# Kernel optimization log

Measured on AMD Instinct MI355X. Metric: run time of the kernel, lower is better.

## Reference

```python
import jax, jax.numpy as jnp
import numpy as np

B, NPG, FANOUT = 32, 1024, 4       # graphs, nodes per graph, tree fan-out
H = 128                            # x_size == h_size
NUM_LAYERS = 4
A, BCAPS = 8, 8                    # TreeCaps a, b
DCC, N_CLASSES = 16, 50
ROUTING_ITER = 3
TYPE_VOCAB, TOKEN_VOCAB = 1000, 30000
EPS = 1e-10


def _build_forest():
    # parent of node i (i>0) is (i-1)//FANOUT; node 0 is root. Same tree per graph.
    child = np.arange(1, NPG)
    parent = (child - 1) // FANOUT
    pos = ((child - 1) % FANOUT).astype(np.float32)           # position in parent's mailbox
    cnt = np.bincount(parent, minlength=NPG).astype(np.float32)
    k = cnt[parent]                                           # child count of each edge's parent
    denom = np.maximum(k - 1.0, 1.0)
    lw = np.where(k == 1.0, 1.0, (k - 1.0 - pos) / denom).astype(np.float32)
    rw = np.where(k == 1.0, 0.0, pos / denom).astype(np.float32)
    offs = (np.arange(B) * NPG)[:, None]
    src = (child[None, :] + offs).reshape(-1).astype(np.int32)
    dst = (parent[None, :] + offs).reshape(-1).astype(np.int32)
    return src, dst, np.tile(lw, B), np.tile(rw, B), np.tile(cnt > 0, B)


def setup_inputs() -> dict:
    key = jax.random.key(0)
    ks = jax.random.split(key, 9)
    src, dst, lw, rw, has_children = _build_forest()
    N = B * NPG
    u = lambda k, s: jax.random.uniform(k, s, jnp.float32, -0.1, 0.1)
    return {
        "type_ids": jax.random.randint(ks[0], (N,), 0, TYPE_VOCAB, dtype=jnp.int32),
        "token_ids": jax.random.randint(ks[1], (N,), 0, TOKEN_VOCAB, dtype=jnp.int32),
        "src": jnp.asarray(src), "dst": jnp.asarray(dst),
        "lw": jnp.asarray(lw), "rw": jnp.asarray(rw),
        "has_children": jnp.asarray(has_children),
        "type_emb": jax.random.normal(ks[2], (TYPE_VOCAB, H - H // 2), jnp.float32),
        "token_emb": jax.random.normal(ks[3], (TOKEN_VOCAB, H // 2), jnp.float32),
        "W_left": u(ks[4], (NUM_LAYERS, H, H)),
        "W_right": u(ks[5], (NUM_LAYERS, H, H)),
        "W_top": u(ks[6], (NUM_LAYERS, H, H)),
        "b_conv": u(ks[7], (NUM_LAYERS, H)),
        "Wjm": 0.01 * jax.random.normal(ks[8], (A * H, DCC, N_CLASSES, NUM_LAYERS), jnp.float32),
    }


def squash(x, axis=-1):
    sq = jnp.sum(x * x, axis=axis, keepdims=True)
    return x * (sq / (1.0 + sq) / (jnp.sqrt(sq + EPS) + 1e-8))


def _vts_routing(uu):
    # uu: [NPG, H, L]  (one graph's primary capsules)
    l2 = jnp.sum(uu.reshape(NPG, -1) ** 2, axis=1)
    _, top_b = jax.lax.top_k(l2, BCAPS)
    u_i = jax.lax.stop_gradient(uu[top_b].reshape(-1, NUM_LAYERS))  # [BCAPS*H, L]
    _, top_a = jax.lax.top_k(l2, A)
    v_j = uu[top_a].reshape(-1, NUM_LAYERS)                         # [A*H, L]
    alpha = jnp.zeros((BCAPS * H, A * H), uu.dtype)
    for _ in range(ROUTING_ITER):
        alpha = alpha + u_i @ v_j.T
        beta = jax.nn.softmax(alpha, axis=-1)
        v_j = beta.T @ u_i
    return squash(v_j)                                              # [A*H, L]


def _dynamic_routing(SC, Wjm):
    # SC: [B, A*H, L], Wjm: [A*H, DCC, S, L]
    v = jnp.einsum('ncsm,bnm->bnsc', Wjm, SC)
    v_stop = jax.lax.stop_gradient(v)
    delta = jnp.zeros(SC.shape[:2] + (N_CLASSES,), SC.dtype)
    z = None
    for r in range(ROUTING_ITER):
        gamma = jax.nn.softmax(delta, axis=-1)
        vv = v if r == ROUTING_ITER - 1 else v_stop
        z = squash(jnp.einsum('bns,bnsc->bsc', gamma, vv))
        if r < ROUTING_ITER - 1:
            delta = delta + jnp.einsum('bnsc,bsc->bns', v_stop, z)
    return z                                                        # [B, S, DCC]


def reference(type_ids, token_ids, src, dst, lw, rw, has_children,
              type_emb, token_emb, W_left, W_right, W_top, b_conv, Wjm):
    h = jnp.concatenate([type_emb[type_ids], token_emb[token_ids]], axis=1)  # [N, H]
    N = h.shape[0]
    feats = []
    for l in range(NUM_LAYERS):
        ch = h[src]                                                 # [E, H] gather children
        msg = (ch @ W_left[l]) * lw[:, None] + (ch @ W_right[l]) * rw[:, None]
        children = jax.ops.segment_sum(msg, dst, num_segments=N)
        new_h = jax.nn.relu(children + h @ W_top[l] + b_conv[l][None, :])
        h = jnp.where(has_children[:, None], new_h, h)              # leaves keep old h
        feats.append(h)
    layer_feats = jnp.stack(feats, axis=-1)                         # [N, H, L]
    SC = jax.vmap(_vts_routing)(layer_feats.reshape(B, NPG, H, NUM_LAYERS))
    z = _dynamic_routing(SC, Wjm)
    logit = jnp.sqrt(jnp.sum(z * z, axis=-1) + EPS)                 # [B, S]
    return (logit, logit)
```

## Files before the change

### kernel.cpp

```cpp
#include <hip/hip_runtime.h>


#define BG      32
#define NPG     1024
#define HH      128
#define NLAY    4
#define INT_PG  256
#define M_INT   8192
#define NN      32768
#define EPG     1023
#define DCC     16
#define NS      50

__global__ void k_embed(const int* __restrict__ tids, const int* __restrict__ kids,
                        const float* __restrict__ temb, const float* __restrict__ kemb,
                        float* __restrict__ h) {
  int idx = blockIdx.x * 256 + threadIdx.x;
  int n = idx >> 5, c4 = idx & 31;
  float4 v;
  if (c4 < 16) v = *(const float4*)(temb + tids[n] * 64 + c4 * 4);
  else         v = *(const float4*)(kemb + kids[n] * 64 + (c4 - 16) * 4);
  *(float4*)(h + n * 128 + c4 * 4) = v;
}

__global__ void k_gather(const float* __restrict__ h, const int* __restrict__ src,
                         const float* __restrict__ lw, const float* __restrict__ rw,
                         float* __restrict__ hl, float* __restrict__ hr) {
  int idx = blockIdx.x * 256 + threadIdx.x;
  int p = idx >> 5, c4 = idx & 31;
  int g = p >> 8, pl = p & 255;
  float4 al = make_float4(0.f, 0.f, 0.f, 0.f);
  float4 ar = make_float4(0.f, 0.f, 0.f, 0.f);
  for (int j = 0; j < 4; ++j) {
    int cc = 4 * pl + 1 + j;
    if (cc < NPG) {
      int e = g * EPG + cc - 1;
      int child = src[e];
      float lv = lw[e], rv = rw[e];
      float4 hv = *(const float4*)(h + child * 128 + c4 * 4);
      al.x = fmaf(lv, hv.x, al.x); al.y = fmaf(lv, hv.y, al.y);
      al.z = fmaf(lv, hv.z, al.z); al.w = fmaf(lv, hv.w, al.w);
      ar.x = fmaf(rv, hv.x, ar.x); ar.y = fmaf(rv, hv.y, ar.y);
      ar.z = fmaf(rv, hv.z, ar.z); ar.w = fmaf(rv, hv.w, ar.w);
    }
  }
  *(float4*)(hl + p * 128 + c4 * 4) = al;
  *(float4*)(hr + p * 128 + c4 * 4) = ar;
}

__global__ __launch_bounds__(256) void k_conv(
    const float* __restrict__ hl, const float* __restrict__ hr,
    float* __restrict__ h,
    const float* __restrict__ Wl, const float* __restrict__ Wr,
    const float* __restrict__ Wt, const float* __restrict__ bias,
    float* __restrict__ feat) {
  __shared__ float Ws[32][128];
  __shared__ float AsT[32][40];
  int tid = threadIdx.x;
  int tx = tid & 31, ty = tid >> 5;
  int rowBase = blockIdx.x * 32;
  int nodeBase = ((rowBase >> 8) << 10) + (rowBase & 255);
  float acc[4][4] = {};
  int sr = tid >> 3, sc4 = (tid & 7) * 4;

  for (int kc = 0; kc < 12; ++kc) {
    int ssel = kc >> 2, kcol = (kc & 3) * 32;
    const float* ap = (ssel == 0) ? (hl + rowBase * 128)
                    : (ssel == 1) ? (hr + rowBase * 128)
                                  : (h + nodeBase * 128);
    const float* wsrc = ((ssel == 0) ? Wl : (ssel == 1) ? Wr : Wt) + kcol * 128;
    float4 av = *(const float4*)(ap + sr * 128 + kcol + sc4);
    float4 wv0, wv1, wv2, wv3;
    {
      int f0 = tid, f1 = tid + 256, f2 = tid + 512, f3 = tid + 768;
      wv0 = *(const float4*)(wsrc + (f0 >> 5) * 128 + (f0 & 31) * 4);
      wv1 = *(const float4*)(wsrc + (f1 >> 5) * 128 + (f1 & 31) * 4);
      wv2 = *(const float4*)(wsrc + (f2 >> 5) * 128 + (f2 & 31) * 4);
      wv3 = *(const float4*)(wsrc + (f3 >> 5) * 128 + (f3 & 31) * 4);
    }
    __syncthreads();
    AsT[sc4 + 0][sr] = av.x; AsT[sc4 + 1][sr] = av.y;
    AsT[sc4 + 2][sr] = av.z; AsT[sc4 + 3][sr] = av.w;
    {
      int f0 = tid, f1 = tid + 256, f2 = tid + 512, f3 = tid + 768;
      *(float4*)&Ws[f0 >> 5][(f0 & 31) * 4] = wv0;
      *(float4*)&Ws[f1 >> 5][(f1 & 31) * 4] = wv1;
      *(float4*)&Ws[f2 >> 5][(f2 & 31) * 4] = wv2;
      *(float4*)&Ws[f3 >> 5][(f3 & 31) * 4] = wv3;
    }
    __syncthreads();
    #pragma unroll
    for (int kk = 0; kk < 32; ++kk) {
      float4 wv = *(float4*)&Ws[kk][tx * 4];
      float4 av2 = *(float4*)&AsT[kk][ty * 4];
      float aa[4] = {av2.x, av2.y, av2.z, av2.w};
      float ww[4] = {wv.x, wv.y, wv.z, wv.w};
      #pragma unroll
      for (int i = 0; i < 4; ++i)
        #pragma unroll
        for (int j = 0; j < 4; ++j)
          acc[i][j] = fmaf(aa[i], ww[j], acc[i][j]);
    }
  }
  float4 bv = *(const float4*)(bias + tx * 4);
  float bb[4] = {bv.x, bv.y, bv.z, bv.w};
  #pragma unroll
  for (int i = 0; i < 4; ++i) {
    int r = ty * 4 + i;
    float4 o = make_float4(fmaxf(acc[i][0] + bb[0], 0.f),
                           fmaxf(acc[i][1] + bb[1], 0.f),
                           fmaxf(acc[i][2] + bb[2], 0.f),
                           fmaxf(acc[i][3] + bb[3], 0.f));
    *(float4*)(feat + (rowBase + r) * 128 + tx * 4) = o;
    *(float4*)(h + (nodeBase + r) * 128 + tx * 4) = o;
  }
}

__global__ void k_l2(const float* __restrict__ h, const float* __restrict__ feat,
                     float* __restrict__ l2) {
  int wid = (blockIdx.x * 256 + threadIdx.x) >> 6;
  int lane = threadIdx.x & 63;
  int g = wid >> 10, local = wid & 1023;
  float s = 0.f;
  if (local >= INT_PG) {
    const float* p = h + wid * 128;
    float a = p[lane], b = p[lane + 64];
    s = (a * a + b * b) * 4.f;
  } else {
    int row = (g * INT_PG + local) * 128;
    #pragma unroll
    for (int l = 0; l < 4; ++l) {
      const float* p = feat + l * (M_INT * 128) + row;
      float a = p[lane], b = p[lane + 64];
      s += a * a + b * b;
    }
  }
  #pragma unroll
  for (int off = 32; off; off >>= 1) s += __shfl_down(s, off);
  if (lane == 0) l2[wid] = s;
}

__global__ void k_topk(const float* __restrict__ l2, int* __restrict__ sel) {
  __shared__ unsigned long long keys[1024];
  __shared__ unsigned long long red[256];
  int g = blockIdx.x, tid = threadIdx.x;
  for (int i = tid; i < 1024; i += 256) {
    unsigned vb = __float_as_uint(l2[g * 1024 + i]);
    keys[i] = ((unsigned long long)vb << 32) | (unsigned)(~i);
  }
  __syncthreads();
  for (int r = 0; r < 8; ++r) {
    unsigned long long best = 0ULL;
    for (int i = tid; i < 1024; i += 256) {
      unsigned long long k = keys[i];
      best = (k > best) ? k : best;
    }
    red[tid] = best;
    __syncthreads();
    for (int st = 128; st; st >>= 1) {
      if (tid < st) {
        unsigned long long a = red[tid], b = red[tid + st];
        red[tid] = (b > a) ? b : a;
      }
      __syncthreads();
    }
    if (tid == 0) {
      unsigned long long k = red[0];
      int idx = (int)(~(unsigned)(k & 0xffffffffu));
      sel[g * 8 + r] = idx;
      keys[idx] = 0ULL;
    }
    __syncthreads();
  }
}

__global__ void k_buildU(const float* __restrict__ h, const float* __restrict__ feat,
                         const int* __restrict__ sel,
                         float* __restrict__ U, float* __restrict__ Vsum) {
  int idx = blockIdx.x * 256 + threadIdx.x;
  int g = idx >> 10, rank = (idx >> 7) & 7, hh = idx & 127;
  int local = sel[g * 8 + rank];
  float4 v;
  if (local >= INT_PG) {
    float x = h[(g * NPG + local) * 128 + hh];
    v = make_float4(x, x, x, x);
  } else {
    int row = (g * INT_PG + local) * 128 + hh;
    v.x = feat[row];
    v.y = feat[M_INT * 128 + row];
    v.z = feat[2 * M_INT * 128 + row];
    v.w = feat[3 * M_INT * 128 + row];
  }
  int o = g * 1024 + rank * 128 + hh;
  ((float4*)U)[o] = v;
  ((float4*)Vsum)[o] = v;
}

__global__ __launch_bounds__(1024) void k_vtsA(const float* __restrict__ U,
                                               const float* __restrict__ Vsum,
                                               float* __restrict__ mw, float* __restrict__ sw) {
  __shared__ float4 Vs[1024];
  __shared__ float2 red[1024];
  int g = blockIdx.x >> 3, rb = (blockIdx.x & 7) * 128;
  int tid = threadIdx.x, l = tid & 63, p = tid >> 6;
  Vs[tid] = ((const float4*)Vsum)[g * 1024 + tid];
  __syncthreads();
  float4 u0 = ((const float4*)U)[g * 1024 + rb + l];
  float4 u1 = ((const float4*)U)[g * 1024 + rb + 64 + l];
  int j0 = p * 64;
  float m0 = -3.4e38f, m1 = -3.4e38f;
  for (int j = j0; j < j0 + 64; ++j) {
    float4 v = Vs[j];
    float a0 = u0.x * v.x + u0.y * v.y + u0.z * v.z + u0.w * v.w;
    float a1 = u1.x * v.x + u1.y * v.y + u1.z * v.z + u1.w * v.w;
    m0 = fmaxf(m0, a0); m1 = fmaxf(m1, a1);
  }
  red[tid] = make_float2(m0, m1);
  __syncthreads();
  #pragma unroll
  for (int st = 512; st >= 64; st >>= 1) {
    if (tid < st) {
      float2 a = red[tid], b = red[tid + st];
      red[tid] = make_float2(fmaxf(a.x, b.x), fmaxf(a.y, b.y));
    }
    __syncthreads();
  }
  float2 mm = red[l];
  __syncthreads();
  float s0 = 0.f, s1 = 0.f;
  for (int j = j0; j < j0 + 64; ++j) {
    float4 v = Vs[j];
    float a0 = u0.x * v.x + u0.y * v.y + u0.z * v.z + u0.w * v.w;
    float a1 = u1.x * v.x + u1.y * v.y + u1.z * v.z + u1.w * v.w;
    s0 += __expf(a0 - mm.x);
    s1 += __expf(a1 - mm.y);
  }
  red[tid] = make_float2(s0, s1);
  __syncthreads();
  #pragma unroll
  for (int st = 512; st >= 64; st >>= 1) {
    if (tid < st) {
      float2 a = red[tid], b = red[tid + st];
      red[tid] = make_float2(a.x + b.x, a.y + b.y);
    }
    __syncthreads();
  }
  if (tid < 64) {
    float2 ss = red[tid];
    mw[g * 1024 + rb + tid] = mm.x;
    mw[g * 1024 + rb + 64 + tid] = mm.y;
    sw[g * 1024 + rb + tid] = ss.x;
    sw[g * 1024 + rb + 64 + tid] = ss.y;
  }
}

__global__ __launch_bounds__(1024) void k_vtsB(const float* __restrict__ U,
                                               float* __restrict__ Vsum,
                                               const float* __restrict__ mw,
                                               const float* __restrict__ sw,
                                               float* __restrict__ SCT, int last) {
  __shared__ float4 Us[1024];
  __shared__ float2 ms[1024];
  __shared__ float4 par[1024];
  int g = blockIdx.x >> 3, cb = (blockIdx.x & 7) * 128;
  int tid = threadIdx.x, l = tid & 63, p = tid >> 6;
  Us[tid] = ((const float4*)U)[g * 1024 + tid];
  ms[tid] = make_float2(mw[g * 1024 + tid], 1.0f / sw[g * 1024 + tid]);
  __syncthreads();
  float4 v0 = ((const float4*)Vsum)[g * 1024 + cb + l];
  float4 v1 = ((const float4*)Vsum)[g * 1024 + cb + 64 + l];
  float4 acc0 = make_float4(0.f, 0.f, 0.f, 0.f);
  float4 acc1 = make_float4(0.f, 0.f, 0.f, 0.f);
  int i0 = p * 64;
  for (int i = i0; i < i0 + 64; ++i) {
    float4 uu = Us[i];
    float2 st = ms[i];
    float a0 = uu.x * v0.x + uu.y * v0.y + uu.z * v0.z + uu.w * v0.w;
    float a1 = uu.x * v1.x + uu.y * v1.y + uu.z * v1.z + uu.w * v1.w;
    float w0 = __expf(a0 - st.x) * st.y;
    float w1 = __expf(a1 - st.x) * st.y;
    acc0.x = fmaf(w0, uu.x, acc0.x); acc0.y = fmaf(w0, uu.y, acc0.y);
    acc0.z = fmaf(w0, uu.z, acc0.z); acc0.w = fmaf(w0, uu.w, acc0.w);
    acc1.x = fmaf(w1, uu.x, acc1.x); acc1.y = fmaf(w1, uu.y, acc1.y);
    acc1.z = fmaf(w1, uu.z, acc1.z); acc1.w = fmaf(w1, uu.w, acc1.w);
  }
  par[tid] = acc0;
  __syncthreads();
  #pragma unroll
  for (int st = 512; st >= 64; st >>= 1) {
    if (tid < st) {
      float4 a = par[tid], b = par[tid + st];
      par[tid] = make_float4(a.x + b.x, a.y + b.y, a.z + b.z, a.w + b.w);
    }
    __syncthreads();
  }
  float4 o0;
  if (tid < 64) o0 = par[tid];
  __syncthreads();
  par[tid] = acc1;
  __syncthreads();
  #pragma unroll
  for (int st = 512; st >= 64; st >>= 1) {
    if (tid < st) {
      float4 a = par[tid], b = par[tid + st];
      par[tid] = make_float4(a.x + b.x, a.y + b.y, a.z + b.z, a.w + b.w);
    }
    __syncthreads();
  }
  if (tid < 64) {
    float4 o1 = par[tid];
    int j0c = cb + tid, j1c = cb + 64 + tid;
    if (last) {
      float sq0 = o0.x * o0.x + o0.y * o0.y + o0.z * o0.z + o0.w * o0.w;
      float f0 = (sq0 / (1.f + sq0)) / (sqrtf(sq0 + 1e-10f) + 1e-8f);
      ((float4*)SCT)[j0c * 32 + g] = make_float4(o0.x * f0, o0.y * f0, o0.z * f0, o0.w * f0);
      float sq1 = o1.x * o1.x + o1.y * o1.y + o1.z * o1.z + o1.w * o1.w;
      float f1 = (sq1 / (1.f + sq1)) / (sqrtf(sq1 + 1e-10f) + 1e-8f);
      ((float4*)SCT)[j1c * 32 + g] = make_float4(o1.x * f1, o1.y * f1, o1.z * f1, o1.w * f1);
    } else {
      float4 w0 = ((const float4*)Vsum)[g * 1024 + j0c];
      float4 w1 = ((const float4*)Vsum)[g * 1024 + j1c];
      ((float4*)Vsum)[g * 1024 + j0c] = make_float4(w0.x + o0.x, w0.y + o0.y,
                                                    w0.z + o0.z, w0.w + o0.w);
      ((float4*)Vsum)[g * 1024 + j1c] = make_float4(w1.x + o1.x, w1.y + o1.y,
                                                    w1.z + o1.z, w1.w + o1.w);
    }
  }
}

__global__ void k_transW(const float* __restrict__ Wjm, float* __restrict__ WT) {
  __shared__ float w[3200];
  int n = blockIdx.x, tid = threadIdx.x;
  for (int i = tid; i < 3200; i += 256) w[i] = Wjm[n * 3200 + i];
  __syncthreads();
  for (int i = tid; i < 3200; i += 256) {
    int s = i >> 6, cm = i & 63, cc = cm >> 2, m = cm & 3;
    WT[(s * 1024 + n) * 64 + cm] = w[(cc * NS + s) * 4 + m];
  }
}

__global__ void k_gamma(const float* __restrict__ delta, float* __restrict__ gT) {
  int idx = blockIdx.x * 256 + threadIdx.x;
  int b = idx & 31, n = idx >> 5;
  const float* dp = delta + n * 32 + b;
  float m = -3.4e38f;
  for (int s = 0; s < NS; ++s) m = fmaxf(m, dp[s * 32768]);
  float sum = 0.f;
  for (int s = 0; s < NS; ++s) sum += __expf(dp[s * 32768] - m);
  float inv = 1.0f / sum;
  float* gp = gT + n * 32 + b;
  for (int s = 0; s < NS; ++s) gp[s * 32768] = __expf(dp[s * 32768] - m) * inv;
}

__global__ __launch_bounds__(256) void k_zsweep(const float* __restrict__ WT,
                                                const float* __restrict__ SCT,
                                                const float* __restrict__ gT,
                                                float* __restrict__ accZ, int it0) {
  int sb = blockIdx.x >> 3, nb = blockIdx.x & 7;
  int tid = threadIdx.x;
  int b = tid & 31, ch = tid >> 5;
  int n0 = nb * 128;
  const float4* wt = (const float4*)WT + (sb * 1024 + n0) * 16;
  const float4* sct = (const float4*)SCT + n0 * 32 + b;
  const float* gp = gT + (sb * 1024 + n0) * 32 + b;
  float a0 = 0.f, a1 = 0.f;
  for (int nn = 0; nn < 128; ++nn) {
    float4 w0 = wt[nn * 16 + ch];
    float4 w1 = wt[nn * 16 + ch + 8];
    float4 s4 = sct[nn * 32];
    float gm = it0 ? (1.0f / 50.0f) : gp[nn * 32];
    float t0 = w0.x * s4.x + w0.y * s4.y + w0.z * s4.z + w0.w * s4.w;
    float t1 = w1.x * s4.x + w1.y * s4.y + w1.z * s4.z + w1.w * s4.w;
    a0 = fmaf(gm, t0, a0);
    a1 = fmaf(gm, t1, a1);
  }
  atomicAdd(accZ + (b * NS + sb) * 16 + ch, a0);
  atomicAdd(accZ + (b * NS + sb) * 16 + ch + 8, a1);
}

__global__ void k_squash(const float* __restrict__ accZ, float* __restrict__ z,
                         float* __restrict__ out, int fin) {
  int idx = blockIdx.x * 256 + threadIdx.x;
  if (idx >= 1600) return;
  const float4* a4 = (const float4*)accZ + idx * 4;
  float4 u0 = a4[0], u1 = a4[1], u2 = a4[2], u3 = a4[3];
  float sq = u0.x * u0.x + u0.y * u0.y + u0.z * u0.z + u0.w * u0.w
           + u1.x * u1.x + u1.y * u1.y + u1.z * u1.z + u1.w * u1.w
           + u2.x * u2.x + u2.y * u2.y + u2.z * u2.z + u2.w * u2.w
           + u3.x * u3.x + u3.y * u3.y + u3.z * u3.z + u3.w * u3.w;
  float f = (sq / (1.f + sq)) / (sqrtf(sq + 1e-10f) + 1e-8f);
  if (fin) {
    float lg = sqrtf(sq * f * f + 1e-10f);
    out[idx] = lg;
    out[idx + 1600] = lg;
  } else {
    float4* z4 = (float4*)z + idx * 4;
    z4[0] = make_float4(u0.x * f, u0.y * f, u0.z * f, u0.w * f);
    z4[1] = make_float4(u1.x * f, u1.y * f, u1.z * f, u1.w * f);
    z4[2] = make_float4(u2.x * f, u2.y * f, u2.z * f, u2.w * f);
    z4[3] = make_float4(u3.x * f, u3.y * f, u3.z * f, u3.w * f);
  }
}

__global__ __launch_bounds__(256) void k_dsweep(const float* __restrict__ WT,
                                                const float* __restrict__ SCT,
                                                const float* __restrict__ z,
                                                float* __restrict__ delta, int first) {
  __shared__ float wl[50 * 64];
  __shared__ float4 scl[32];
  int n = blockIdx.x;
  int tid = threadIdx.x;
  for (int i = tid; i < 3200; i += 256)
    wl[i] = WT[((i >> 6) * 1024 + n) * 64 + (i & 63)];
  if (tid < 32) scl[tid] = ((const float4*)SCT)[n * 32 + tid];
  __syncthreads();
  for (int idx = tid; idx < 1600; idx += 256) {
    int s = idx >> 5, b = idx & 31;
    const float4* wp = (const float4*)(wl + s * 64);
    const float4* zp = (const float4*)(z + (b * 50 + s) * 16);
    float4 z0 = zp[0], z1 = zp[1], z2 = zp[2], z3 = zp[3];
    float zs[16] = {z0.x, z0.y, z0.z, z0.w, z1.x, z1.y, z1.z, z1.w,
                    z2.x, z2.y, z2.z, z2.w, z3.x, z3.y, z3.z, z3.w};
    float4 y = make_float4(0.f, 0.f, 0.f, 0.f);
    #pragma unroll
    for (int c = 0; c < 16; ++c) {
      float4 w = wp[c];
      float zc = zs[c];
      y.x = fmaf(zc, w.x, y.x); y.y = fmaf(zc, w.y, y.y);
      y.z = fmaf(zc, w.z, y.z); y.w = fmaf(zc, w.w, y.w);
    }
    float4 sc = scl[b];
    float dd = sc.x * y.x + sc.y * y.y + sc.z * y.z + sc.w * y.w;
    float* dp = delta + (s * 1024 + n) * 32 + b;
    if (first) *dp = dd; else *dp = *dp + dd;
  }
}

extern "C" void kernel_launch(void* const* d_in, const int* in_sizes, int n_in,
                              void* d_out, int out_size, void* d_ws, size_t ws_size,
                              hipStream_t stream) {
  const int*   type_ids  = (const int*)d_in[0];
  const int*   token_ids = (const int*)d_in[1];
  const int*   src       = (const int*)d_in[2];
  const float* lw        = (const float*)d_in[4];
  const float* rw        = (const float*)d_in[5];
  const float* temb      = (const float*)d_in[7];
  const float* kemb      = (const float*)d_in[8];
  const float* Wl        = (const float*)d_in[9];
  const float* Wr        = (const float*)d_in[10];
  const float* Wt        = (const float*)d_in[11];
  const float* bconv     = (const float*)d_in[12];
  const float* Wjm       = (const float*)d_in[13];
  float* out = (float*)d_out;
  char* wsb = (char*)d_ws;

  float* h     = (float*)(wsb + 0);
  float* WT    = (float*)(wsb + 0);
  float* feat  = (float*)(wsb + 16777216);
  float* gT    = (float*)(wsb + 16777216);
  float* delta = (float*)(wsb + 23330816);
  float* accZ  = (float*)(wsb + 29884416);
  float* zbuf  = (float*)(wsb + 29986816);
  float* hl    = (float*)(wsb + 33554432);
  float* hr    = (float*)(wsb + 37748736);
  float* l2b   = (float*)(wsb + 33554432);
  int*   sel   = (int*)  (wsb + 33685504);
  float* U     = (float*)(wsb + 33686528);
  float* Vsum  = (float*)(wsb + 34210816);
  float* mw    = (float*)(wsb + 34735104);
  float* sw    = (float*)(wsb + 34866176);
  float* SCT   = (float*)(wsb + 34997248);

  k_embed<<<4096, 256, 0, stream>>>(type_ids, token_ids, temb, kemb, h);

  for (int l = 0; l < NLAY; ++l) {
    k_gather<<<1024, 256, 0, stream>>>(h, src, lw, rw, hl, hr);
    k_conv<<<256, 256, 0, stream>>>(hl, hr, h,
                                    Wl + l * 16384, Wr + l * 16384, Wt + l * 16384,
                                    bconv + l * 128, feat + l * (M_INT * 128));
  }

  k_l2<<<8192, 256, 0, stream>>>(h, feat, l2b);
  k_topk<<<32, 256, 0, stream>>>(l2b, sel);
  k_buildU<<<128, 256, 0, stream>>>(h, feat, sel, U, Vsum);
  k_transW<<<1024, 256, 0, stream>>>(Wjm, WT);

  for (int it = 0; it < 3; ++it) {
    k_vtsA<<<256, 1024, 0, stream>>>(U, Vsum, mw, sw);
    k_vtsB<<<256, 1024, 0, stream>>>(U, Vsum, mw, sw, SCT, it == 2 ? 1 : 0);
  }

  for (int it = 0; it < 3; ++it) {
    if (it > 0) k_gamma<<<128, 256, 0, stream>>>(delta, gT);
    hipMemsetAsync(accZ, 0, 32 * 50 * 16 * 4, stream);
    k_zsweep<<<400, 256, 0, stream>>>(WT, SCT, gT, accZ, it == 0 ? 1 : 0);
    k_squash<<<7, 256, 0, stream>>>(accZ, zbuf, out, it == 2 ? 1 : 0);
    if (it < 2) k_dsweep<<<1024, 256, 0, stream>>>(WT, SCT, zbuf, delta, it == 0 ? 1 : 0);
  }
}
```

Before: 518.9 us.

## Fuse pipeline into three persistent kernels with software grid barriers

Replaces roughly twenty kernel launches with three persistent kernels: tree conv plus top-k selection, VTS routing, and dynamic routing. Stages are separated by atomic-counter grid barriers instead of launch boundaries. The child gather is fused into the conv kernel, which keeps weighted child sums in registers and drops the hl/hr intermediate buffers and the src indirection. This removes launch overhead and intermediate global traffic, but relies on every block being co-resident, and the spin barriers can serialize work or deadlock if occupancy is insufficient.

Measured after the change: 1.401 ms. 2.7x slower.

```diff
diff --git a/kernel.cpp b/kernel.cpp
--- a/kernel.cpp
+++ b/kernel.cpp
@@ -3,436 +3,475 @@
 
 #define BG      32
 #define NPG     1024
-#define HH      128
 #define NLAY    4
 #define INT_PG  256
 #define M_INT   8192
 #define NN      32768
 #define EPG     1023
-#define DCC     16
 #define NS      50
 
-__global__ void k_embed(const int* __restrict__ tids, const int* __restrict__ kids,
-                        const float* __restrict__ temb, const float* __restrict__ kemb,
-                        float* __restrict__ h) {
-  int idx = blockIdx.x * 256 + threadIdx.x;
-  int n = idx >> 5, c4 = idx & 31;
-  float4 v;
-  if (c4 < 16) v = *(const float4*)(temb + tids[n] * 64 + c4 * 4);
-  else         v = *(const float4*)(kemb + kids[n] * 64 + (c4 - 16) * 4);
-  *(float4*)(h + n * 128 + c4 * 4) = v;
+__device__ __forceinline__ void gbar(unsigned int* bar, unsigned int target) {
+  __syncthreads();
+  if (threadIdx.x == 0) {
+    __threadfence();
+    __hip_atomic_fetch_add(bar, 1u, __ATOMIC_ACQ_REL, __HIP_MEMORY_SCOPE_AGENT);
+    while (__hip_atomic_load(bar, __ATOMIC_ACQUIRE, __HIP_MEMORY_SCOPE_AGENT) < target)
+      __builtin_amdgcn_s_sleep(1);
+  }
+  __syncthreads();
 }
 
-__global__ void k_gather(const float* __restrict__ h, const int* __restrict__ src,
-                         const float* __restrict__ lw, const float* __restrict__ rw,
-                         float* __restrict__ hl, float* __restrict__ hr) {
-  int idx = blockIdx.x * 256 + threadIdx.x;
-  int p = idx >> 5, c4 = idx & 31;
-  int g = p >> 8, pl = p & 255;
-  float4 al = make_float4(0.f, 0.f, 0.f, 0.f);
-  float4 ar = make_float4(0.f, 0.f, 0.f, 0.f);
-  for (int j = 0; j < 4; ++j) {
-    int cc = 4 * pl + 1 + j;
-    if (cc < NPG) {
-      int e = g * EPG + cc - 1;
-      int child = src[e];
-      float lv = lw[e], rv = rw[e];
-      float4 hv = *(const float4*)(h + child * 128 + c4 * 4);
-      al.x = fmaf(lv, hv.x, al.x); al.y = fmaf(lv, hv.y, al.y);
-      al.z = fmaf(lv, hv.z, al.z); al.w = fmaf(lv, hv.w, al.w);
-      ar.x = fmaf(rv, hv.x, ar.x); ar.y = fmaf(rv, hv.y, ar.y);
-      ar.z = fmaf(rv, hv.z, ar.z); ar.w = fmaf(rv, hv.w, ar.w);
-    }
-  }
-  *(float4*)(hl + p * 128 + c4 * 4) = al;
-  *(float4*)(hr + p * 128 + c4 * 4) = ar;
+__global__ __launch_bounds__(256) void k_mega(
+    const int* __restrict__ tids, const int* __restrict__ kids,
+    const float* __restrict__ temb, const float* __restrict__ kemb,
+    const float* __restrict__ lw, const float* __restrict__ rw,
+    const float* __restrict__ Wl, const float* __restrict__ Wr,
+    const float* __restrict__ Wt, const float* __restrict__ bconv,
+    float* __restrict__ h, float* __restrict__ feat,
+    float* __restrict__ l2b, int* __restrict__ sel,
+    float* __restrict__ U, float* __restrict__ Vsum,
+    unsigned int* __restrict__ bar) {
+  __shared__ union {
+    struct { float Ws[32][128]; float AsT[32][36]; } c;
+    struct { unsigned long long keys[1024]; unsigned long long red[256]; } t;
+  } sm;
+  int tid = threadIdx.x, bid = blockIdx.x;
+  int gtid = bid * 256 + tid;
+  unsigned int bt = 0;
+
+  for (int i = gtid; i < NN * 32; i += 65536) {
+    int n = i >> 5, c4 = i & 31;
+    float4 v;
+    if (c4 < 16) v = *(const float4*)(temb + tids[n] * 64 + c4 * 4);
+    else         v = *(const float4*)(kemb + kids[n] * 64 + (c4 - 16) * 4);
+    *(float4*)(h + n * 128 + c4 * 4) = v;
+  }
+  bt += 256; gbar(bar, bt);
+
+  int rowBase = bid * 32;
+  int g = rowBase >> 8, pb = rowBase & 255;
+  int nodeBase = g * 1024 + pb;
+  int tx = tid & 31, ty = tid >> 5;
+  int p8 = tid >> 3, c16 = (tid & 7) * 16;
+
+  for (int l = 0; l < NLAY; ++l) {
+    float av[16], bv[16], cv[16];
+    {
+      int PL = pb + p8;
+      const float* hp = h + (g * 1024 + PL) * 128 + c16;
+      #pragma unroll
+      for (int q = 0; q < 4; ++q) {
+        float4 t4 = *(const float4*)(hp + q * 4);
+        cv[q*4] = t4.x; cv[q*4+1] = t4.y; cv[q*4+2] = t4.z; cv[q*4+3] = t4.w;
+      }
+      #pragma unroll
+      for (int i = 0; i < 16; ++i) { av[i] = 0.f; bv[i] = 0.f; }
+      for (int j = 0; j < 4; ++j) {
+        int cc = 4 * PL + 1 + j;
+        if (cc < 1024) {
+          int e = g * EPG + cc - 1;
+          float lv = lw[e], rv = rw[e];
+          const float* hc = h + (g * 1024 + cc) * 128 + c16;
+          #pragma unroll
+          for (int q = 0; q < 4; ++q) {
+            float4 t4 = *(const float4*)(hc + q * 4);
+            av[q*4]   = fmaf(lv, t4.x, av[q*4]);   bv[q*4]   = fmaf(rv, t4.x, bv[q*4]);
+            av[q*4+1] = fmaf(lv, t4.y, av[q*4+1]); bv[q*4+1] = fmaf(rv, t4.y, bv[q*4+1]);
+            av[q*4+2] = fmaf(lv, t4.z, av[q*4+2]); bv[q*4+2] = fmaf(rv, t4.z, bv[q*4+2]);
+            av[q*4+3] = fmaf(lv, t4.w, av[q*4+3]); bv[q*4+3] = fmaf(rv, t4.w, bv[q*4+3]);
+          }
+        }
+      }
+    }
+    bt += 256; gbar(bar, bt);
+
+    const float* WlL = Wl + l * 16384;
+    const float* WrL = Wr + l * 16384;
+    const float* WtL = Wt + l * 16384;
+    float acc[4][4] = {};
+    for (int kc = 0; kc < 12; ++kc) {
+      int ssel = kc >> 2, koff = (kc & 3) * 32;
+      const float* wsrc = ((ssel == 0) ? WlL : (ssel == 1) ? WrL : WtL) + koff * 128;
+      float4 wv0, wv1, wv2, wv3;
+      {
+        int f0 = tid, f1 = tid + 256, f2 = tid + 512, f3 = tid + 768;
+        wv0 = *(const float4*)(wsrc + (f0 >> 5) * 128 + (f0 & 31) * 4);
+        wv1 = *(const float4*)(wsrc + (f1 >> 5) * 128 + (f1 & 31) * 4);
+        wv2 = *(const float4*)(wsrc + (f2 >> 5) * 128 + (f2 & 31) * 4);
+        wv3 = *(const float4*)(wsrc + (f3 >> 5) * 128 + (f3 & 31) * 4);
+      }
+      __syncthreads();
+      {
+        int f0 = tid, f1 = tid + 256, f2 = tid + 512, f3 = tid + 768;
+        *(float4*)&sm.c.Ws[f0 >> 5][(f0 & 31) * 4] = wv0;
+        *(float4*)&sm.c.Ws[f1 >> 5][(f1 & 31) * 4] = wv1;
+        *(float4*)&sm.c.Ws[f2 >> 5][(f2 & 31) * 4] = wv2;
+        *(float4*)&sm.c.Ws[f3 >> 5][(f3 & 31) * 4] = wv3;
+      }
+      int rel = (tid & 7) - ((kc & 3) << 1);
+      if (rel == 0 || rel == 1) {
+        int kk0 = rel << 4;
+        if (ssel == 0) {
+          #pragma unroll
+          for (int i = 0; i < 16; ++i) sm.c.AsT[kk0 + i][p8] = av[i];
+        } else if (ssel == 1) {
+          #pragma unroll
+          for (int i = 0; i < 16; ++i) sm.c.AsT[kk0 + i][p8] = bv[i];
+        } else {
+          #pragma unroll
+          for (int i = 0; i < 16; ++i) sm.c.AsT[kk0 + i][p8] = cv[i];
+        }
+      }
+      __syncthreads();
+      #pragma unroll
+      for (int kk = 0; kk < 32; ++kk) {
+        float4 wv = *(float4*)&sm.c.Ws[kk][tx * 4];
+        float4 av2 = *(float4*)&sm.c.AsT[kk][ty * 4];
+        float aa[4] = {av2.x, av2.y, av2.z, av2.w};
+        float ww[4] = {wv.x, wv.y, wv.z, wv.w};
+        #pragma unroll
+        for (int i = 0; i < 4; ++i)
+          #pragma unroll
+          for (int j = 0; j < 4; ++j)
+            acc[i][j] = fmaf(aa[i], ww[j], acc[i][j]);
+      }
+    }
+    float4 bv4 = *(const float4*)(bconv + l * 128 + tx * 4);
+    float bb[4] = {bv4.x, bv4.y, bv4.z, bv4.w};
+    float* featL = feat + l * (M_INT * 128);
+    #pragma unroll
+    for (int i = 0; i < 4; ++i) {
+      int r = ty * 4 + i;
+      float4 o = make_float4(fmaxf(acc[i][0] + bb[0], 0.f),
+                             fmaxf(acc[i][1] + bb[1], 0.f),
+                             fmaxf(acc[i][2] + bb[2], 0.f),
+                             fmaxf(acc[i][3] + bb[3], 0.f));
+      *(float4*)(featL + (rowBase + r) * 128 + tx * 4) = o;
+      *(float4*)(h + (nodeBase + r) * 128 + tx * 4) = o;
+    }
+    bt += 256; gbar(bar, bt);
+  }
+
+  {
+    int w = bid * 4 + (tid >> 6);
+    int lane = tid & 63;
+    for (int gg = 0; gg < 32; ++gg) {
+      int nd = gg * 1024 + w;
+      float s = 0.f;
+      if (w >= INT_PG) {
+        const float* p = h + nd * 128;
+        float a = p[lane], b = p[lane + 64];
+        s = (a * a + b * b) * 4.f;
+      } else {
+        int row = (gg * INT_PG + w) * 128;
+        #pragma unroll
+        for (int l = 0; l < 4; ++l) {
+          const float* p = feat + l * (M_INT * 128) + row;
+          float a = p[lane], b = p[lane + 64];
+          s += a * a + b * b;
+        }
+      }
+      #pragma unroll
+      for (int off = 32; off; off >>= 1) s += __shfl_down(s, off);
+      if (lane == 0) l2b[nd] = s;
+    }
+  }
+  bt += 256; gbar(bar, bt);
+
+  if (bid < 32) {
+    int gg = bid;
+    for (int i = tid; i < 1024; i += 256) {
+      unsigned vb = __float_as_uint(l2b[gg * 1024 + i]);
+      sm.t.keys[i] = ((unsigned long long)vb << 32) | (unsigned)(~i);
+    }
+    __syncthreads();
+    for (int r = 0; r < 8; ++r) {
+      unsigned long long best = 0ULL;
+      for (int i = tid; i < 1024; i += 256) {
+        unsigned long long k = sm.t.keys[i];
+        best = (k > best) ? k : best;
+      }
+      sm.t.red[tid] = best;
+      __syncthreads();
+      for (int st = 128; st; st >>= 1) {
+        if (tid < st) {
+          unsigned long long a = sm.t.red[tid], b = sm.t.red[tid + st];
+          sm.t.red[tid] = (b > a) ? b : a;
+        }
+        __syncthreads();
+      }
+      if (tid == 0) {
+        unsigned long long k = sm.t.red[0];
+        int idx = (int)(~(unsigned)(k & 0xffffffffu));
+        sel[gg * 8 + r] = idx;
+        sm.t.keys[idx] = 0ULL;
+      }
+      __syncthreads();
+    }
+  }
+  bt += 256; gbar(bar, bt);
+
+  if (gtid < 32768) {
+    int gg = gtid >> 10, rank = (gtid >> 7) & 7, hh = gtid & 127;
+    int local = sel[gg * 8 + rank];
+    float4 v;
+    if (local >= INT_PG) {
+      float x = h[(gg * NPG + local) * 128 + hh];
+      v = make_float4(x, x, x, x);
+    } else {
+      int row = (gg * INT_PG + local) * 128 + hh;
+      v.x = feat[row];
+      v.y = feat[M_INT * 128 + row];
+      v.z = feat[2 * M_INT * 128 + row];
+      v.w = feat[3 * M_INT * 128 + row];
+    }
+    int o = gg * 1024 + rank * 128 + hh;
+    ((float4*)U)[o] = v;
+    ((float4*)Vsum)[o] = v;
+  }
 }
 
-__global__ __launch_bounds__(256) void k_conv(
-    const float* __restrict__ hl, const float* __restrict__ hr,
-    float* __restrict__ h,
-    const float* __restrict__ Wl, const float* __restrict__ Wr,
-    const float* __restrict__ Wt, const float* __restrict__ bias,
-    float* __restrict__ feat) {
-  __shared__ float Ws[32][128];
-  __shared__ float AsT[32][40];
-  int tid = threadIdx.x;
-  int tx = tid & 31, ty = tid >> 5;
-  int rowBase = blockIdx.x * 32;
-  int nodeBase = ((rowBase >> 8) << 10) + (rowBase & 255);
-  float acc[4][4] = {};
-  int sr = tid >> 3, sc4 = (tid & 7) * 4;
-
-  for (int kc = 0; kc < 12; ++kc) {
-    int ssel = kc >> 2, kcol = (kc & 3) * 32;
-    const float* ap = (ssel == 0) ? (hl + rowBase * 128)
-                    : (ssel == 1) ? (hr + rowBase * 128)
-                                  : (h + nodeBase * 128);
-    const float* wsrc = ((ssel == 0) ? Wl : (ssel == 1) ? Wr : Wt) + kcol * 128;
-    float4 av = *(const float4*)(ap + sr * 128 + kcol + sc4);
-    float4 wv0, wv1, wv2, wv3;
+__global__ __launch_bounds__(1024) void k_vts(
+    const float* __restrict__ U, float* __restrict__ Vsum,
+    float* __restrict__ mw, float* __restrict__ sw, float* __restrict__ SCT,
+    unsigned int* __restrict__ bar) {
+  __shared__ union {
+    struct { float4 Vs[1024]; float2 red[1024]; } a;
+    struct { float4 Us[1024]; float2 ms[1024]; float4 par[1024]; } b;
+  } s;
+  int g = blockIdx.x >> 3, blk = (blockIdx.x & 7) * 128;
+  int tid = threadIdx.x, l = tid & 63, p = tid >> 6;
+  unsigned int bt = 0;
+
+  for (int it = 0; it < 3; ++it) {
+    s.a.Vs[tid] = ((const float4*)Vsum)[g * 1024 + tid];
+    __syncthreads();
+    float4 u0 = ((const float4*)U)[g * 1024 + blk + l];
+    float4 u1 = ((const float4*)U)[g * 1024 + blk + 64 + l];
+    int j0 = p * 64;
+    float m0 = -3.4e38f, m1 = -3.4e38f;
+    for (int j = j0; j < j0 + 64; ++j) {
+      float4 v = s.a.Vs[j];
+      float a0 = u0.x * v.x + u0.y * v.y + u0.z * v.z + u0.w * v.w;
+      float a1 = u1.x * v.x + u1.y * v.y + u1.z * v.z + u1.w * v.w;
+      m0 = fmaxf(m0, a0); m1 = fmaxf(m1, a1);
+    }
+    s.a.red[tid] = make_float2(m0, m1);
+    __syncthreads();
+    #pragma unroll
+    for (int st = 512; st >= 64; st >>= 1) {
+      if (tid < st) {
+        float2 a = s.a.red[tid], b = s.a.red[tid + st];
+        s.a.red[tid] = make_float2(fmaxf(a.x, b.x), fmaxf(a.y, b.y));
+      }
+      __syncthreads();
+    }
+    float2 mm = s.a.red[l];
+    __syncthreads();
+    float s0 = 0.f, s1 = 0.f;
+    for (int j = j0; j < j0 + 64; ++j) {
+      float4 v = s.a.Vs[j];
+      float a0 = u0.x * v.x + u0.y * v.y + u0.z * v.z + u0.w * v.w;
+      float a1 = u1.x * v.x + u1.y * v.y + u1.z * v.z + u1.w * v.w;
+      s0 += __expf(a0 - mm.x);
+      s1 += __expf(a1 - mm.y);
+    }
+    s.a.red[tid] = make_float2(s0, s1);
+    __syncthreads();
+    #pragma unroll
+    for (int st = 512; st >= 64; st >>= 1) {
+      if (tid < st) {
+        float2 a = s.a.red[tid], b = s.a.red[tid + st];
+        s.a.red[tid] = make_float2(a.x + b.x, a.y + b.y);
+      }
+      __syncthreads();
+    }
+    if (tid < 64) {
+      float2 ss = s.a.red[tid];
+      mw[g * 1024 + blk + tid] = mm.x;
+      mw[g * 1024 + blk + 64 + tid] = mm.y;
+      sw[g * 1024 + blk + tid] = ss.x;
+      sw[g * 1024 + blk + 64 + tid] = ss.y;
+    }
+    bt += 256; gbar(bar, bt);
+
+    s.b.Us[tid] = ((const float4*)U)[g * 1024 + tid];
+    s.b.ms[tid] = make_float2(mw[g * 1024 + tid], 1.0f / sw[g * 1024 + tid]);
+    __syncthreads();
+    float4 v0 = ((const float4*)Vsum)[g * 1024 + blk + l];
+    float4 v1 = ((const float4*)Vsum)[g * 1024 + blk + 64 + l];
+    float4 acc0 = make_float4(0.f, 0.f, 0.f, 0.f);
+    float4 acc1 = make_float4(0.f, 0.f, 0.f, 0.f);
+    int i0 = p * 64;
+    for (int i = i0; i < i0 + 64; ++i) {
+      float4 uu = s.b.Us[i];
+      float2 st2 = s.b.ms[i];
+      float a0 = uu.x * v0.x + uu.y * v0.y + uu.z * v0.z + uu.w * v0.w;
+      float a1 = uu.x * v1.x + uu.y * v1.y + uu.z * v1.z + uu.w * v1.w;
+      float w0 = __expf(a0 - st2.x) * st2.y;
+      float w1 = __expf(a1 - st2.x) * st2.y;
+      acc0.x = fmaf(w0, uu.x, acc0.x); acc0.y = fmaf(w0, uu.y, acc0.y);
+      acc0.z = fmaf(w0, uu.z, acc0.z); acc0.w = fmaf(w0, uu.w, acc0.w);
+      acc1.x = fmaf(w1, uu.x, acc1.x); acc1.y = fmaf(w1, uu.y, acc1.y);
+      acc1.z = fmaf(w1, uu.z, acc1.z); acc1.w = fmaf(w1, uu.w, acc1.w);
+    }
+    s.b.par[tid] = acc0;
+    __syncthreads();
+    #pragma unroll
+    for (int st = 512; st >= 64; st >>= 1) {
+      if (tid < st) {
+        float4 a = s.b.par[tid], b = s.b.par[tid + st];
+        s.b.par[tid] = make_float4(a.x + b.x, a.y + b.y, a.z + b.z, a.w + b.w);
+      }
+      __syncthreads();
+    }
+    float4 o0 = make_float4(0.f, 0.f, 0.f, 0.f);
+    if (tid < 64) o0 = s.b.par[tid];
+    __syncthreads();
+    s.b.par[tid] = acc1;
+    __syncthreads();
+    #pragma unroll
+    for (int st = 512; st >= 64; st >>= 1) {
+      if (tid < st) {
+        float4 a = s.b.par[tid], b = s.b.par[tid + st];
+        s.b.par[tid] = make_float4(a.x + b.x, a.y + b.y, a.z + b.z, a.w + b.w);
+      }
+      __syncthreads();
+    }
+    if (tid < 64) {
+      float4 o1 = s.b.par[tid];
+      int j0c = blk + tid, j1c = blk + 64 + tid;
+      if (it == 2) {
+        float sq0 = o0.x * o0.x + o0.y * o0.y + o0.z * o0.z + o0.w * o0.w;
+        float f0 = (sq0 / (1.f + sq0)) / (sqrtf(sq0 + 1e-10f) + 1e-8f);
+        ((float4*)SCT)[j0c * 32 + g] = make_float4(o0.x * f0, o0.y * f0, o0.z * f0, o0.w * f0);
+        float sq1 = o1.x * o1.x + o1.y * o1.y + o1.z * o1.z + o1.w * o1.w;
+        float f1 = (sq1 / (1.f + sq1)) / (sqrtf(sq1 + 1e-10f) + 1e-8f);
+        ((float4*)SCT)[j1c * 32 + g] = make_float4(o1.x * f1, o1.y * f1, o1.z * f1, o1.w * f1);
+      } else {
+        float4 w0 = ((const float4*)Vsum)[g * 1024 + j0c];
+        float4 w1 = ((const float4*)Vsum)[g * 1024 + j1c];
+        ((float4*)Vsum)[g * 1024 + j0c] = make_float4(w0.x + o0.x, w0.y + o0.y,
+                                                      w0.z + o0.z, w0.w + o0.w);
+        ((float4*)Vsum)[g * 1024 + j1c] = make_float4(w1.x + o1.x, w1.y + o1.y,
+                                                      w1.z + o1.z, w1.w + o1.w);
+      }
+    }
+    if (it < 2) { bt += 256; gbar(bar, bt); }
+  }
+}
+
+__global__ __launch_bounds__(256) void k_route(
+    const float* __restrict__ Wjm, float* __restrict__ WT,
+    const float* __restrict__ SCT, float* __restrict__ gT,
+    float* __restrict__ delta, float* __restrict__ accZ0,
+    float* __restrict__ accZ1, float* __restrict__ zbuf,
+    float* __restrict__ out, unsigned int* __restrict__ bar) {
+  __shared__ float4 wl4[2048];
+  __shared__ float zl[512];
+  int tid = threadIdx.x, bid = blockIdx.x;
+  int gtid = bid * 256 + tid;
+  unsigned int bt = 0;
+
+  {
+    float* wtr = (float*)wl4;
+    for (int n = bid; n < 1024; n += 400) {
+      for (int i = tid; i < 3200; i += 256) wtr[i] = Wjm[n * 3200 + i];
+      __syncthreads();
+      for (int i = tid; i < 3200; i += 256) {
+        int s = i >> 6, cm = i & 63, cc = cm >> 2, m = cm & 3;
+        WT[(s * 1024 + n) * 64 + cm] = wtr[(cc * NS + s) * 4 + m];
+      }
+      __syncthreads();
+    }
+  }
+  if (gtid < 6400) {
+    float4 z4 = make_float4(0.f, 0.f, 0.f, 0.f);
+    ((float4*)accZ0)[gtid] = z4;
+    ((float4*)accZ1)[gtid] = z4;
+  }
+  bt += 400; gbar(bar, bt);
+
+  int sb = bid >> 3, nb = bid & 7, n0 = nb * 128;
+  for (int i = tid; i < 2048; i += 256)
+    wl4[i] = ((const float4*)WT)[(sb * 1024 + n0) * 16 + i];
+  __syncthreads();
+  int b = tid & 31, ch = tid >> 5;
+
+  for (int it = 0; it < 3; ++it) {
+    float* accC = (it & 1) ? accZ1 : accZ0;
+    float* accO = (it & 1) ? accZ0 : accZ1;
     {
-      int f0 = tid, f1 = tid + 256, f2 = tid + 512, f3 = tid + 768;
-      wv0 = *(const float4*)(wsrc + (f0 >> 5) * 128 + (f0 & 31) * 4);
-      wv1 = *(const float4*)(wsrc + (f1 >> 5) * 128 + (f1 & 31) * 4);
-      wv2 = *(const float4*)(wsrc + (f2 >> 5) * 128 + (f2 & 31) * 4);
-      wv3 = *(const float4*)(wsrc + (f3 >> 5) * 128 + (f3 & 31) * 4);
-    }
-    __syncthreads();
-    AsT[sc4 + 0][sr] = av.x; AsT[sc4 + 1][sr] = av.y;
-    AsT[sc4 + 2][sr] = av.z; AsT[sc4 + 3][sr] = av.w;
-    {
-      int f0 = tid, f1 = tid + 256, f2 = tid + 512, f3 = tid + 768;
-      *(float4*)&Ws[f0 >> 5][(f0 & 31) * 4] = wv0;
-      *(float4*)&Ws[f1 >> 5][(f1 & 31) * 4] = wv1;
-      *(float4*)&Ws[f2 >> 5][(f2 & 31) * 4] = wv2;
-      *(float4*)&Ws[f3 >> 5][(f3 & 31) * 4] = wv3;
-    }
-    __syncthreads();
-    #pragma unroll
-    for (int kk = 0; kk < 32; ++kk) {
-      float4 wv = *(float4*)&Ws[kk][tx * 4];
-      float4 av2 = *(float4*)&AsT[kk][ty * 4];
-      float aa[4] = {av2.x, av2.y, av2.z, av2.w};
-      float ww[4] = {wv.x, wv.y, wv.z, wv.w};
+      const float4* sct = (const float4*)SCT + n0 * 32 + b;
+      const float* gp = gT + (sb * 1024 + n0) * 32 + b;
+      float a0 = 0.f, a1 = 0.f;
+      for (int nn = 0; nn < 128; ++nn) {
+        float4 w0 = wl4[nn * 16 + ch];
+        float4 w1 = wl4[nn * 16 + ch + 8];
+        float4 s4 = sct[nn * 32];
+        float gm = (it == 0) ? 0.02f : gp[nn * 32];
+        float t0 = w0.x * s4.x + w0.y * s4.y + w0.z * s4.z + w0.w * s4.w;
+        float t1 = w1.x * s4.x + w1.y * s4.y + w1.z * s4.z + w1.w * s4.w;
+        a0 = fmaf(gm, t0, a0);
+        a1 = fmaf(gm, t1, a1);
+      }
+      atomicAdd(accC + (b * NS + sb) * 16 + ch, a0);
+      atomicAdd(accC + (b * NS + sb) * 16 + ch + 8, a1);
+      if (gtid < 25600) accO[gtid] = 0.f;
+    }
+    bt += 400; gbar(bar, bt);
+    if (gtid < 1600) {
+      const float4* a4 = (const float4*)accC + gtid * 4;
+      float4 u0 = a4[0], u1 = a4[1], u2 = a4[2], u3 = a4[3];
+      float sq = u0.x*u0.x + u0.y*u0.y + u0.z*u0.z + u0.w*u0.w
+               + u1.x*u1.x + u1.y*u1.y + u1.z*u1.z + u1.w*u1.w
+               + u2.x*u2.x + u2.y*u2.y + u2.z*u2.z + u2.w*u2.w
+               + u3.x*u3.x + u3.y*u3.y + u3.z*u3.z + u3.w*u3.w;
+      float f = (sq / (1.f + sq)) / (sqrtf(sq + 1e-10f) + 1e-8f);
+      if (it == 2) {
+        float lg = sqrtf(sq * f * f + 1e-10f);
+        out[gtid] = lg;
+        out[gtid + 1600] = lg;
+      } else {
+        float4* z4 = (float4*)zbuf + gtid * 4;
+        z4[0] = make_float4(u0.x * f, u0.y * f, u0.z * f, u0.w * f);
+        z4[1] = make_float4(u1.x * f, u1.y * f, u1.z * f, u1.w * f);
+        z4[2] = make_float4(u2.x * f, u2.y * f, u2.z * f, u2.w * f);
+        z4[3] = make_float4(u3.x * f, u3.y * f, u3.z * f, u3.w * f);
+      }
+    }
+    if (it == 2) break;
+    bt += 400; gbar(bar, bt);
+    for (int i = tid; i < 512; i += 256) {
+      int c = i >> 5, bb = i & 31;
+      zl[c * 32 + bb] = zbuf[bb * 800 + sb * 16 + c];
+    }
+    __syncthreads();
+    for (int item = tid; item < 4096; item += 256) {
+      int nn = item >> 5, bb = item & 31;
+      float4 sc4 = ((const float4*)SCT)[(n0 + nn) * 32 + bb];
+      float dd = 0.f;
       #pragma unroll
-      for (int i = 0; i < 4; ++i)
-        #pragma unroll
-        for (int j = 0; j < 4; ++j)
-          acc[i][j] = fmaf(aa[i], ww[j], acc[i][j]);
-    }
-  }
-  float4 bv = *(const float4*)(bias + tx * 4);
-  float bb[4] = {bv.x, bv.y, bv.z, bv.w};
-  #pragma unroll
-  for (int i = 0; i < 4; ++i) {
-    int r = ty * 4 + i;
-    float4 o = make_float4(fmaxf(acc[i][0] + bb[0], 0.f),
-                           fmaxf(acc[i][1] + bb[1], 0.f),
-                           fmaxf(acc[i][2] + bb[2], 0.f),
-                           fmaxf(acc[i][3] + bb[3], 0.f));
-    *(float4*)(feat + (rowBase + r) * 128 + tx * 4) = o;
-    *(float4*)(h + (nodeBase + r) * 128 + tx * 4) = o;
-  }
-}
-
-__global__ void k_l2(const float* __restrict__ h, const float* __restrict__ feat,
-                     float* __restrict__ l2) {
-  int wid = (blockIdx.x * 256 + threadIdx.x) >> 6;
-  int lane = threadIdx.x & 63;
-  int g = wid >> 10, local = wid & 1023;
-  float s = 0.f;
-  if (local >= INT_PG) {
-    const float* p = h + wid * 128;
-    float a = p[lane], b = p[lane + 64];
-    s = (a * a + b * b) * 4.f;
-  } else {
-    int row = (g * INT_PG + local) * 128;
-    #pragma unroll
-    for (int l = 0; l < 4; ++l) {
-      const float* p = feat + l * (M_INT * 128) + row;
-      float a = p[lane], b = p[lane + 64];
-      s += a * a + b * b;
-    }
-  }
-  #pragma unroll
-  for (int off = 32; off; off >>= 1) s += __shfl_down(s, off);
-  if (lane == 0) l2[wid] = s;
-}
-
-__global__ void k_topk(const float* __restrict__ l2, int* __restrict__ sel) {
-  __shared__ unsigned long long keys[1024];
-  __shared__ unsigned long long red[256];
-  int g = blockIdx.x, tid = threadIdx.x;
-  for (int i = tid; i < 1024; i += 256) {
-    unsigned vb = __float_as_uint(l2[g * 1024 + i]);
-    keys[i] = ((unsigned long long)vb << 32) | (unsigned)(~i);
-  }
-  __syncthreads();
-  for (int r = 0; r < 8; ++r) {
-    unsigned long long best = 0ULL;
-    for (int i = tid; i < 1024; i += 256) {
-      unsigned long long k = keys[i];
-      best = (k > best) ? k : best;
-    }
-    red[tid] = best;
-    __syncthreads();
-    for (int st = 128; st; st >>= 1) {
-      if (tid < st) {
-        unsigned long long a = red[tid], b = red[tid + st];
-        red[tid] = (b > a) ? b : a;
-      }
-      __syncthreads();
-    }
-    if (tid == 0) {
-      unsigned long long k = red[0];
-      int idx = (int)(~(unsigned)(k & 0xffffffffu));
-      sel[g * 8 + r] = idx;
-      keys[idx] = 0ULL;
-    }
-    __syncthreads();
-  }
-}
-
-__global__ void k_buildU(const float* __restrict__ h, const float* __restrict__ feat,
-                         const int* __restrict__ sel,
-                         float* __restrict__ U, float* __restrict__ Vsum) {
-  int idx = blockIdx.x * 256 + threadIdx.x;
-  int g = idx >> 10, rank = (idx >> 7) & 7, hh = idx & 127;
-  int local = sel[g * 8 + rank];
-  float4 v;
-  if (local >= INT_PG) {
-    float x = h[(g * NPG + local) * 128 + hh];
-    v = make_float4(x, x, x, x);
-  } else {
-    int row = (g * INT_PG + local) * 128 + hh;
-    v.x = feat[row];
-    v.y = feat[M_INT * 128 + row];
-    v.z = feat[2 * M_INT * 128 + row];
-    v.w = feat[3 * M_INT * 128 + row];
-  }
-  int o = g * 1024 + rank * 128 + hh;
-  ((float4*)U)[o] = v;
-  ((float4*)Vsum)[o] = v;
-}
-
-__global__ __launch_bounds__(1024) void k_vtsA(const float* __restrict__ U,
-                                               const float* __restrict__ Vsum,
-                                               float* __restrict__ mw, float* __restrict__ sw) {
-  __shared__ float4 Vs[1024];
-  __shared__ float2 red[1024];
-  int g = blockIdx.x >> 3, rb = (blockIdx.x & 7) * 128;
-  int tid = threadIdx.x, l = tid & 63, p = tid >> 6;
-  Vs[tid] = ((const float4*)Vsum)[g * 1024 + tid];
-  __syncthreads();
-  float4 u0 = ((const float4*)U)[g * 1024 + rb + l];
-  float4 u1 = ((const float4*)U)[g * 1024 + rb + 64 + l];
-  int j0 = p * 64;
-  float m0 = -3.4e38f, m1 = -3.4e38f;
-  for (int j = j0; j < j0 + 64; ++j) {
-    float4 v = Vs[j];
-    float a0 = u0.x * v.x + u0.y * v.y + u0.z * v.z + u0.w * v.w;
-    float a1 = u1.x * v.x + u1.y * v.y + u1.z * v.z + u1.w * v.w;
-    m0 = fmaxf(m0, a0); m1 = fmaxf(m1, a1);
-  }
-  red[tid] = make_float2(m0, m1);
-  __syncthreads();
-  #pragma unroll
-  for (int st = 512; st >= 64; st >>= 1) {
-    if (tid < st) {
-      float2 a = red[tid], b = red[tid + st];
-      red[tid] = make_float2(fmaxf(a.x, b.x), fmaxf(a.y, b.y));
-    }
-    __syncthreads();
-  }
-  float2 mm = red[l];
-  __syncthreads();
-  float s0 = 0.f, s1 = 0.f;
-  for (int j = j0; j < j0 + 64; ++j) {
-    float4 v = Vs[j];
-    float a0 = u0.x * v.x + u0.y * v.y + u0.z * v.z + u0.w * v.w;
-    float a1 = u1.x * v.x + u1.y * v.y + u1.z * v.z + u1.w * v.w;
-    s0 += __expf(a0 - mm.x);
-    s1 += __expf(a1 - mm.y);
-  }
-  red[tid] = make_float2(s0, s1);
-  __syncthreads();
-  #pragma unroll
-  for (int st = 512; st >= 64; st >>= 1) {
-    if (tid < st) {
-      float2 a = red[tid], b = red[tid + st];
-      red[tid] = make_float2(a.x + b.x, a.y + b.y);
-    }
-    __syncthreads();
-  }
-  if (tid < 64) {
-    float2 ss = red[tid];
-    mw[g * 1024 + rb + tid] = mm.x;
-    mw[g * 1024 + rb + 64 + tid] = mm.y;
-    sw[g * 1024 + rb + tid] = ss.x;
-    sw[g * 1024 + rb + 64 + tid] = ss.y;
-  }
-}
-
-__global__ __launch_bounds__(1024) void k_vtsB(const float* __restrict__ U,
-                                               float* __restrict__ Vsum,
-                                               const float* __restrict__ mw,
-                                               const float* __restrict__ sw,
-                                               float* __restrict__ SCT, int last) {
-  __shared__ float4 Us[1024];
-  __shared__ float2 ms[1024];
-  __shared__ float4 par[1024];
-  int g = blockIdx.x >> 3, cb = (blockIdx.x & 7) * 128;
-  int tid = threadIdx.x, l = tid & 63, p = tid >> 6;
-  Us[tid] = ((const float4*)U)[g * 1024 + tid];
-  ms[tid] = make_float2(mw[g * 1024 + tid], 1.0f / sw[g * 1024 + tid]);
-  __syncthreads();
-  float4 v0 = ((const float4*)Vsum)[g * 1024 + cb + l];
-  float4 v1 = ((const float4*)Vsum)[g * 1024 + cb + 64 + l];
-  float4 acc0 = make_float4(0.f, 0.f, 0.f, 0.f);
-  float4 acc1 = make_float4(0.f, 0.f, 0.f, 0.f);
-  int i0 = p * 64;
-  for (int i = i0; i < i0 + 64; ++i) {
-    float4 uu = Us[i];
-    float2 st = ms[i];
-    float a0 = uu.x * v0.x + uu.y * v0.y + uu.z * v0.z + uu.w * v0.w;
-    float a1 = uu.x * v1.x + uu.y * v1.y + uu.z * v1.z + uu.w * v1.w;
-    float w0 = __expf(a0 - st.x) * st.y;
-    float w1 = __expf(a1 - st.x) * st.y;
-    acc0.x = fmaf(w0, uu.x, acc0.x); acc0.y = fmaf(w0, uu.y, acc0.y);
-    acc0.z = fmaf(w0, uu.z, acc0.z); acc0.w = fmaf(w0, uu.w, acc0.w);
-    acc1.x = fmaf(w1, uu.x, acc1.x); acc1.y = fmaf(w1, uu.y, acc1.y);
-    acc1.z = fmaf(w1, uu.z, acc1.z); acc1.w = fmaf(w1, uu.w, acc1.w);
-  }
-  par[tid] = acc0;
-  __syncthreads();
-  #pragma unroll
-  for (int st = 512; st >= 64; st >>= 1) {
-    if (tid < st) {
-      float4 a = par[tid], b = par[tid + st];
-      par[tid] = make_float4(a.x + b.x, a.y + b.y, a.z + b.z, a.w + b.w);
-    }
-    __syncthreads();
-  }
-  float4 o0;
-  if (tid < 64) o0 = par[tid];
-  __syncthreads();
-  par[tid] = acc1;
-  __syncthreads();
-  #pragma unroll
-  for (int st = 512; st >= 64; st >>= 1) {
-    if (tid < st) {
-      float4 a = par[tid], b = par[tid + st];
-      par[tid] = make_float4(a.x + b.x, a.y + b.y, a.z + b.z, a.w + b.w);
-    }
-    __syncthreads();
-  }
-  if (tid < 64) {
-    float4 o1 = par[tid];
-    int j0c = cb + tid, j1c = cb + 64 + tid;
-    if (last) {
-      float sq0 = o0.x * o0.x + o0.y * o0.y + o0.z * o0.z + o0.w * o0.w;
-      float f0 = (sq0 / (1.f + sq0)) / (sqrtf(sq0 + 1e-10f) + 1e-8f);
-      ((float4*)SCT)[j0c * 32 + g] = make_float4(o0.x * f0, o0.y * f0, o0.z * f0, o0.w * f0);
-      float sq1 = o1.x * o1.x + o1.y * o1.y + o1.z * o1.z + o1.w * o1.w;
-      float f1 = (sq1 / (1.f + sq1)) / (sqrtf(sq1 + 1e-10f) + 1e-8f);
-      ((float4*)SCT)[j1c * 32 + g] = make_float4(o1.x * f1, o1.y * f1, o1.z * f1, o1.w * f1);
-    } else {
-      float4 w0 = ((const float4*)Vsum)[g * 1024 + j0c];
-      float4 w1 = ((const float4*)Vsum)[g * 1024 + j1c];
-      ((float4*)Vsum)[g * 1024 + j0c] = make_float4(w0.x + o0.x, w0.y + o0.y,
-                                                    w0.z + o0.z, w0.w + o0.w);
-      ((float4*)Vsum)[g * 1024 + j1c] = make_float4(w1.x + o1.x, w1.y + o1.y,
-                                                    w1.z + o1.z, w1.w + o1.w);
-    }
-  }
-}
-
-__global__ void k_transW(const float* __restrict__ Wjm, float* __restrict__ WT) {
-  __shared__ float w[3200];
-  int n = blockIdx.x, tid = threadIdx.x;
-  for (int i = tid; i < 3200; i += 256) w[i] = Wjm[n * 3200 + i];
-  __syncthreads();
-  for (int i = tid; i < 3200; i += 256) {
-    int s = i >> 6, cm = i & 63, cc = cm >> 2, m = cm & 3;
-    WT[(s * 1024 + n) * 64 + cm] = w[(cc * NS + s) * 4 + m];
-  }
-}
-
-__global__ void k_gamma(const float* __restrict__ delta, float* __restrict__ gT) {
-  int idx = blockIdx.x * 256 + threadIdx.x;
-  int b = idx & 31, n = idx >> 5;
-  const float* dp = delta + n * 32 + b;
-  float m = -3.4e38f;
-  for (int s = 0; s < NS; ++s) m = fmaxf(m, dp[s * 32768]);
-  float sum = 0.f;
-  for (int s = 0; s < NS; ++s) sum += __expf(dp[s * 32768] - m);
-  float inv = 1.0f / sum;
-  float* gp = gT + n * 32 + b;
-  for (int s = 0; s < NS; ++s) gp[s * 32768] = __expf(dp[s * 32768] - m) * inv;
-}
-
-__global__ __launch_bounds__(256) void k_zsweep(const float* __restrict__ WT,
-                                                const float* __restrict__ SCT,
-                                                const float* __restrict__ gT,
-                                                float* __restrict__ accZ, int it0) {
-  int sb = blockIdx.x >> 3, nb = blockIdx.x & 7;
-  int tid = threadIdx.x;
-  int b = tid & 31, ch = tid >> 5;
-  int n0 = nb * 128;
-  const float4* wt = (const float4*)WT + (sb * 1024 + n0) * 16;
-  const float4* sct = (const float4*)SCT + n0 * 32 + b;
-  const float* gp = gT + (sb * 1024 + n0) * 32 + b;
-  float a0 = 0.f, a1 = 0.f;
-  for (int nn = 0; nn < 128; ++nn) {
-    float4 w0 = wt[nn * 16 + ch];
-    float4 w1 = wt[nn * 16 + ch + 8];
-    float4 s4 = sct[nn * 32];
-    float gm = it0 ? (1.0f / 50.0f) : gp[nn * 32];
-    float t0 = w0.x * s4.x + w0.y * s4.y + w0.z * s4.z + w0.w * s4.w;
-    float t1 = w1.x * s4.x + w1.y * s4.y + w1.z * s4.z + w1.w * s4.w;
-    a0 = fmaf(gm, t0, a0);
-    a1 = fmaf(gm, t1, a1);
-  }
-  atomicAdd(accZ + (b * NS + sb) * 16 + ch, a0);
-  atomicAdd(accZ + (b * NS + sb) * 16 + ch + 8, a1);
-}
-
-__global__ void k_squash(const float* __restrict__ accZ, float* __restrict__ z,
-                         float* __restrict__ out, int fin) {
-  int idx = blockIdx.x * 256 + threadIdx.x;
-  if (idx >= 1600) return;
-  const float4* a4 = (const float4*)accZ + idx * 4;
-  float4 u0 = a4[0], u1 = a4[1], u2 = a4[2], u3 = a4[3];
-  float sq = u0.x * u0.x + u0.y * u0.y + u0.z * u0.z + u0.w * u0.w
-           + u1.x * u1.x + u1.y * u1.y + u1.z * u1.z + u1.w * u1.w
-           + u2.x * u2.x + u2.y * u2.y + u2.z * u2.z + u2.w * u2.w
-           + u3.x * u3.x + u3.y * u3.y + u3.z * u3.z + u3.w * u3.w;
-  float f = (sq / (1.f + sq)) / (sqrtf(sq + 1e-10f) + 1e-8f);
-  if (fin) {
-    float lg = sqrtf(sq * f * f + 1e-10f);
-    out[idx] = lg;
-    out[idx + 1600] = lg;
-  } else {
-    float4* z4 = (float4*)z + idx * 4;
-    z4[0] = make_float4(u0.x * f, u0.y * f, u0.z * f, u0.w * f);
-    z4[1] = make_float4(u1.x * f, u1.y * f, u1.z * f, u1.w * f);
-    z4[2] = make_float4(u2.x * f, u2.y * f, u2.z * f, u2.w * f);
-    z4[3] = make_float4(u3.x * f, u3.y * f, u3.z * f, u3.w * f);
-  }
-}
-
-__global__ __launch_bounds__(256) void k_dsweep(const float* __restrict__ WT,
-                                                const float* __restrict__ SCT,
-                                                const float* __restrict__ z,
-                                                float* __restrict__ delta, int first) {
-  __shared__ float wl[50 * 64];
-  __shared__ float4 scl[32];
-  int n = blockIdx.x;
-  int tid = threadIdx.x;
-  for (int i = tid; i < 3200; i += 256)
-    wl[i] = WT[((i >> 6) * 1024 + n) * 64 + (i & 63)];
-  if (tid < 32) scl[tid] = ((const float4*)SCT)[n * 32 + tid];
-  __syncthreads();
-  for (int idx = tid; idx < 1600; idx += 256) {
-    int s = idx >> 5, b = idx & 31;
-    const float4* wp = (const float4*)(wl + s * 64);
-    const float4* zp = (const float4*)(z + (b * 50 + s) * 16);
-    float4 z0 = zp[0], z1 = zp[1], z2 = zp[2], z3 = zp[3];
-    float zs[16] = {z0.x, z0.y, z0.z, z0.w, z1.x, z1.y, z1.z, z1.w,
-                    z2.x, z2.y, z2.z, z2.w, z3.x, z3.y, z3.z, z3.w};
-    float4 y = make_float4(0.f, 0.f, 0.f, 0.f);
-    #pragma unroll
-    for (int c = 0; c < 16; ++c) {
-      float4 w = wp[c];
-      float zc = zs[c];
-      y.x = fmaf(zc, w.x, y.x); y.y = fmaf(zc, w.y, y.y);
-      y.z = fmaf(zc, w.z, y.z); y.w = fmaf(zc, w.w, y.w);
-    }
-    float4 sc = scl[b];
-    float dd = sc.x * y.x + sc.y * y.y + sc.z * y.z + sc.w * y.w;
-    float* dp = delta + (s * 1024 + n) * 32 + b;
-    if (first) *dp = dd; else *dp = *dp + dd;
+      for (int c = 0; c < 16; ++c) {
+        float4 w = wl4[nn * 16 + c];
+        float y = w.x * sc4.x + w.y * sc4.y + w.z * sc4.z + w.w * sc4.w;
+        dd = fmaf(zl[c * 32 + bb], y, dd);
+      }
+      float* dp = delta + (sb * 1024 + n0 + nn) * 32 + bb;
+      if (it == 0) *dp = dd; else *dp = *dp + dd;
+    }
+    bt += 400; gbar(bar, bt);
+    if (gtid < 32768) {
+      const float* dp = delta + gtid;
+      float m = -3.4e38f;
+      for (int s = 0; s < NS; ++s) m = fmaxf(m, dp[s * 32768]);
+      float sum = 0.f;
+      for (int s = 0; s < NS; ++s) sum += __expf(dp[s * 32768] - m);
+      float inv = 1.0f / sum;
+      float* gq = gT + gtid;
+      for (int s = 0; s < NS; ++s) gq[s * 32768] = __expf(dp[s * 32768] - m) * inv;
+    }
+    bt += 400; gbar(bar, bt);
   }
 }
 
@@ -441,7 +480,6 @@
                               hipStream_t stream) {
   const int*   type_ids  = (const int*)d_in[0];
   const int*   token_ids = (const int*)d_in[1];
-  const int*   src       = (const int*)d_in[2];
   const float* lw        = (const float*)d_in[4];
   const float* rw        = (const float*)d_in[5];
   const float* temb      = (const float*)d_in[7];
@@ -459,10 +497,9 @@
   float* feat  = (float*)(wsb + 16777216);
   float* gT    = (float*)(wsb + 16777216);
   float* delta = (float*)(wsb + 23330816);
-  float* accZ  = (float*)(wsb + 29884416);
+  float* accZ0 = (float*)(wsb + 29884416);
   float* zbuf  = (float*)(wsb + 29986816);
-  float* hl    = (float*)(wsb + 33554432);
-  float* hr    = (float*)(wsb + 37748736);
+  float* accZ1 = (float*)(wsb + 30089216);
   float* l2b   = (float*)(wsb + 33554432);
   int*   sel   = (int*)  (wsb + 33685504);
   float* U     = (float*)(wsb + 33686528);
@@ -470,31 +507,16 @@
   float* mw    = (float*)(wsb + 34735104);
   float* sw    = (float*)(wsb + 34866176);
   float* SCT   = (float*)(wsb + 34997248);
-
-  k_embed<<<4096, 256, 0, stream>>>(type_ids, token_ids, temb, kemb, h);
-
-  for (int l = 0; l < NLAY; ++l) {
-    k_gather<<<1024, 256, 0, stream>>>(h, src, lw, rw, hl, hr);
-    k_conv<<<256, 256, 0, stream>>>(hl, hr, h,
-                                    Wl + l * 16384, Wr + l * 16384, Wt + l * 16384,
-                                    bconv + l * 128, feat + l * (M_INT * 128));
-  }
-
-  k_l2<<<8192, 256, 0, stream>>>(h, feat, l2b);
-  k_topk<<<32, 256, 0, stream>>>(l2b, sel);
-  k_buildU<<<128, 256, 0, stream>>>(h, feat, sel, U, Vsum);
-  k_transW<<<1024, 256, 0, stream>>>(Wjm, WT);
-
-  for (int it = 0; it < 3; ++it) {
-    k_vtsA<<<256, 1024, 0, stream>>>(U, Vsum, mw, sw);
-    k_vtsB<<<256, 1024, 0, stream>>>(U, Vsum, mw, sw, SCT, it == 2 ? 1 : 0);
-  }
-
-  for (int it = 0; it < 3; ++it) {
-    if (it > 0) k_gamma<<<128, 256, 0, stream>>>(delta, gT);
-    hipMemsetAsync(accZ, 0, 32 * 50 * 16 * 4, stream);
-    k_zsweep<<<400, 256, 0, stream>>>(WT, SCT, gT, accZ, it == 0 ? 1 : 0);
-    k_squash<<<7, 256, 0, stream>>>(accZ, zbuf, out, it == 2 ? 1 : 0);
-    if (it < 2) k_dsweep<<<1024, 256, 0, stream>>>(WT, SCT, zbuf, delta, it == 0 ? 1 : 0);
-  }
+  unsigned int* bar0 = (unsigned int*)(wsb + 35521536);
+  unsigned int* bar1 = (unsigned int*)(wsb + 35521536 + 64);
+  unsigned int* bar2 = (unsigned int*)(wsb + 35521536 + 128);
+
+  hipMemsetAsync(wsb + 35521536, 0, 192, stream);
+
+  k_mega<<<256, 256, 0, stream>>>(type_ids, token_ids, temb, kemb, lw, rw,
+                                  Wl, Wr, Wt, bconv, h, feat, l2b, sel,
+                                  U, Vsum, bar0);
+  k_vts<<<256, 1024, 0, stream>>>(U, Vsum, mw, sw, SCT, bar1);
+  k_route<<<400, 256, 0, stream>>>(Wjm, WT, SCT, gT, delta, accZ0, accZ1,
+                                   zbuf, out, bar2);
 }
```
